# Kernel tuning notes

Measured on AMD Instinct MI355X. Metric: run time of the kernel, lower is better.

The kernel has to match this reference:

```python
import jax, jax.numpy as jnp
import numpy as np

N_NODES = 100000


def high_pass_filter(z, src, dst, n):
    # add self loops (PyG add_self_loops appends [i, i] edges)
    loop = jnp.arange(n, dtype=src.dtype)
    src2 = jnp.concatenate([src, loop])
    dst2 = jnp.concatenate([dst, loop])
    ones = jnp.ones(src2.shape[0], dtype=z.dtype)
    # deg = degree(edge_index[0]) -> out-degree counts per source node
    deg = jax.ops.segment_sum(ones, src2, num_segments=n)
    # mean aggregation at target nodes: out[i] = mean_{(j->i)} z[j]
    msg_sum = jax.ops.segment_sum(z[src2], dst2, num_segments=n)
    cnt = jax.ops.segment_sum(ones, dst2, num_segments=n)
    mean_out = msg_sum / cnt[:, None]  # cnt >= 1 thanks to self loops
    return z - mean_out / deg[:, None]


def setup_inputs() -> dict:
    key = jax.random.key(0)
    k = jax.random.split(key, 8)
    d = 64
    E = 1200000
    x = jax.random.normal(k[0], (N_NODES, d), dtype=jnp.float32)
    edge_index = jax.random.randint(k[1], (2, E), 0, N_NODES, dtype=jnp.int64)
    s = 1.0 / np.sqrt(d)
    W1 = jax.random.uniform(k[2], (d, d), jnp.float32, -s, s)
    b1 = jax.random.uniform(k[3], (d,), jnp.float32, -s, s)
    W2 = jax.random.uniform(k[4], (d, d), jnp.float32, -s, s)
    b2 = jax.random.uniform(k[5], (d,), jnp.float32, -s, s)
    W3 = jax.random.uniform(k[6], (d, d), jnp.float32, -s, s)
    b3 = jax.random.uniform(k[7], (d,), jnp.float32, -s, s)
    return {"x": x, "edge_index": edge_index, "W1": W1, "b1": b1,
            "W2": W2, "b2": b2, "W3": W3, "b3": b3}


def reference(x, edge_index, W1, b1, W2, b2, W3, b3):
    src, dst = edge_index[0], edge_index[1]
    n = x.shape[0]
    z = jax.nn.relu(x @ W1 + b1)
    z = high_pass_filter(z, src, dst, n)
    z = jax.nn.relu(z @ W2 + b2)
    z = high_pass_filter(z, src, dst, n)
    z = jax.nn.relu(z @ W3 + b3)
    return z
```

## Files before the change

kernel.cpp:

```cpp
#include <hip/hip_runtime.h>

#define D 64
#define CAP 48
#define CAPB 3584
#define BIN_CHUNK 2048

typedef unsigned int uint;
typedef unsigned short ushort;

__device__ __forceinline__ ushort f2bf(float f) {
    uint u = __float_as_uint(f);
    return (ushort)((u + 0x7FFFu + ((u >> 16) & 1u)) >> 16);
}

__global__ __launch_bounds__(256) void k_bin2(
    const int* __restrict__ src, const int* __restrict__ dst, int E, int nb,
    int* __restrict__ gcur, int* __restrict__ binD, int* __restrict__ binS)
{
    __shared__ int curD[512], curS[512];
    const int t = threadIdx.x;
    for (int i = t; i < nb; i += 256) { curD[i] = 0; curS[i] = 0; }
    __syncthreads();

    const int e0 = blockIdx.x * BIN_CHUNK;
    int sv[8], dv[8];
#pragma unroll
    for (int i = 0; i < 8; ++i) {
        int e = e0 + i * 256 + t;
        if (e < E) {
            sv[i] = src[e]; dv[i] = dst[e];
            atomicAdd(&curD[dv[i] >> 8], 1);
            atomicAdd(&curS[sv[i] >> 8], 1);
        } else {
            sv[i] = -1;
        }
    }
    __syncthreads();
    for (int i = t; i < nb; i += 256) {
        int c = curD[i]; curD[i] = c ? atomicAdd(&gcur[i], c) : 0;
        c = curS[i];     curS[i] = c ? atomicAdd(&gcur[nb + i], c) : 0;
    }
    __syncthreads();
#pragma unroll
    for (int i = 0; i < 8; ++i) {
        if (sv[i] >= 0) {
            int b = dv[i] >> 8;
            int pos = atomicAdd(&curD[b], 1);
            if (pos < CAPB) binD[(size_t)b * CAPB + pos] = ((dv[i] & 255) << 17) | sv[i];
            b = sv[i] >> 8;
            pos = atomicAdd(&curS[b], 1);
            if (pos < CAPB) binS[(size_t)b * CAPB + pos] = sv[i] & 255;
        }
    }
}

__global__ __launch_bounds__(256) void k_finish(
    const int* __restrict__ gcur, const int* __restrict__ binD,
    const int* __restrict__ binS, int n, int nb,
    int* __restrict__ csr, int* __restrict__ icnt, float* __restrict__ inv)
{
    __shared__ int cur[256], od[256];
    const int b = blockIdx.x, t = threadIdx.x;
    cur[t] = 0; od[t] = 0;
    __syncthreads();

    int cntD = gcur[b]; if (cntD > CAPB) cntD = CAPB;
    const int* bb = binD + (size_t)b * CAPB;
    for (int i = t; i < cntD; i += 256) {
        int v = bb[i];
        int dloc = v >> 17;
        int pos = atomicAdd(&cur[dloc], 1);
        if (pos < CAP) csr[(size_t)((b << 8) + dloc) * CAP + pos] = v & 0x1FFFF;
    }
    int cntS = gcur[nb + b]; if (cntS > CAPB) cntS = CAPB;
    const int* bs = binS + (size_t)b * CAPB;
    for (int i = t; i < cntS; i += 256) {
        atomicAdd(&od[bs[i]], 1);
    }
    __syncthreads();
    int node = (b << 8) + t;
    if (node < n) {
        int ic = cur[t]; if (ic > CAP) ic = CAP;
        icnt[node] = ic;
        inv[node] = 1.0f / ((float)(od[t] + 1) * (float)(ic + 1));
    }
}

__global__ __launch_bounds__(256) void k_aggr(
    const float* __restrict__ zA, const ushort* __restrict__ zh,
    const int* __restrict__ icnt, const int* __restrict__ csr,
    const float* __restrict__ inv, int n, float* __restrict__ zB)
{
    int w = (blockIdx.x * 256 + threadIdx.x) >> 6;
    int lane = threadIdx.x & 63;
    int c8 = (lane & 7) << 3;
    int j = lane >> 3;
    if (w >= n) return;

    int cnt = icnt[w]; if (cnt > CAP) cnt = CAP;
    int rs = w * CAP;
    float a[8] = {0.f, 0.f, 0.f, 0.f, 0.f, 0.f, 0.f, 0.f};
    for (int e = rs + j; e < rs + cnt; e += 8) {
        int s = csr[e];
        uint4 u = *(const uint4*)(zh + (size_t)s * D + c8);
        a[0] += __uint_as_float(u.x << 16);
        a[1] += __uint_as_float(u.x & 0xFFFF0000u);
        a[2] += __uint_as_float(u.y << 16);
        a[3] += __uint_as_float(u.y & 0xFFFF0000u);
        a[4] += __uint_as_float(u.z << 16);
        a[5] += __uint_as_float(u.z & 0xFFFF0000u);
        a[6] += __uint_as_float(u.w << 16);
        a[7] += __uint_as_float(u.w & 0xFFFF0000u);
    }
#pragma unroll
    for (int m = 8; m <= 32; m <<= 1) {
#pragma unroll
        for (int i = 0; i < 8; ++i) a[i] += __shfl_xor(a[i], m, 64);
    }

    if (j == 0) {
        float iv = inv[w];
        const float* zr = zA + (size_t)w * D + c8;
        float4 s0 = *(const float4*)zr;
        float4 s1 = *(const float4*)(zr + 4);
        float4 o0, o1;
        o0.x = fmaf(-(a[0] + s0.x), iv, s0.x);
        o0.y = fmaf(-(a[1] + s0.y), iv, s0.y);
        o0.z = fmaf(-(a[2] + s0.z), iv, s0.z);
        o0.w = fmaf(-(a[3] + s0.w), iv, s0.w);
        o1.x = fmaf(-(a[4] + s1.x), iv, s1.x);
        o1.y = fmaf(-(a[5] + s1.y), iv, s1.y);
        o1.z = fmaf(-(a[6] + s1.z), iv, s1.z);
        o1.w = fmaf(-(a[7] + s1.w), iv, s1.w);
        float* zo = zB + (size_t)w * D + c8;
        *(float4*)zo = o0;
        *(float4*)(zo + 4) = o1;
    }
}

#define LDS_STRIDE 68

__global__ __launch_bounds__(256) void k_gemm(
    const float* z, const float* __restrict__ W, const float* __restrict__ bias,
    float* out, ushort* zh_out, int n)
{
    __shared__ float sX[64 * LDS_STRIDE];
    __shared__ float sWT[64 * LDS_STRIDE];

    const int t = threadIdx.x;
    const int row0 = blockIdx.x * 64;

    for (int i = 0; i < 4; ++i) {
        int s = i * 256 + t;
        int k = s >> 4;
        int c4 = (s & 15) << 2;
        float4 w = ((const float4*)W)[s];
        sWT[(c4 + 0) * LDS_STRIDE + k] = w.x;
        sWT[(c4 + 1) * LDS_STRIDE + k] = w.y;
        sWT[(c4 + 2) * LDS_STRIDE + k] = w.z;
        sWT[(c4 + 3) * LDS_STRIDE + k] = w.w;
    }
    for (int i = 0; i < 4; ++i) {
        int s = i * 256 + t;
        int r = s >> 4;
        int grow = row0 + r;
        float4 v = make_float4(0.f, 0.f, 0.f, 0.f);
        if (grow < n) v = ((const float4*)(z + (size_t)grow * D))[s & 15];
        *((float4*)(sX + r * LDS_STRIDE + ((s & 15) << 2))) = v;
    }
    __syncthreads();

    const int tc = (t & 15) << 2;
    const int tr = (t >> 4) << 2;

    float acc[4][4] = {};
#define DOT4(a_, w_, acc_) \
    acc_ = fmaf((a_).x, (w_).x, fmaf((a_).y, (w_).y, fmaf((a_).z, (w_).z, fmaf((a_).w, (w_).w, acc_))))

    for (int k4 = 0; k4 < 16; ++k4) {
        float4 a0 = *(const float4*)(sX + (tr + 0) * LDS_STRIDE + (k4 << 2));
        float4 a1 = *(const float4*)(sX + (tr + 1) * LDS_STRIDE + (k4 << 2));
        float4 a2 = *(const float4*)(sX + (tr + 2) * LDS_STRIDE + (k4 << 2));
        float4 a3 = *(const float4*)(sX + (tr + 3) * LDS_STRIDE + (k4 << 2));
        float4 w0 = *(const float4*)(sWT + (tc + 0) * LDS_STRIDE + (k4 << 2));
        float4 w1 = *(const float4*)(sWT + (tc + 1) * LDS_STRIDE + (k4 << 2));
        float4 w2 = *(const float4*)(sWT + (tc + 2) * LDS_STRIDE + (k4 << 2));
        float4 w3 = *(const float4*)(sWT + (tc + 3) * LDS_STRIDE + (k4 << 2));
        DOT4(a0, w0, acc[0][0]); DOT4(a0, w1, acc[0][1]); DOT4(a0, w2, acc[0][2]); DOT4(a0, w3, acc[0][3]);
        DOT4(a1, w0, acc[1][0]); DOT4(a1, w1, acc[1][1]); DOT4(a1, w2, acc[1][2]); DOT4(a1, w3, acc[1][3]);
        DOT4(a2, w0, acc[2][0]); DOT4(a2, w1, acc[2][1]); DOT4(a2, w2, acc[2][2]); DOT4(a2, w3, acc[2][3]);
        DOT4(a3, w0, acc[3][0]); DOT4(a3, w1, acc[3][1]); DOT4(a3, w2, acc[3][2]); DOT4(a3, w3, acc[3][3]);
    }

    float b0 = bias[tc + 0], b1 = bias[tc + 1], b2 = bias[tc + 2], b3 = bias[tc + 3];
    for (int rr = 0; rr < 4; ++rr) {
        int grow = row0 + tr + rr;
        if (grow >= n) continue;
        float4 o;
        o.x = fmaxf(acc[rr][0] + b0, 0.f);
        o.y = fmaxf(acc[rr][1] + b1, 0.f);
        o.z = fmaxf(acc[rr][2] + b2, 0.f);
        o.w = fmaxf(acc[rr][3] + b3, 0.f);
        ((float4*)(out + (size_t)grow * D))[tc >> 2] = o;
        if (zh_out) {
            short4 h;
            h.x = (short)f2bf(o.x); h.y = (short)f2bf(o.y);
            h.z = (short)f2bf(o.z); h.w = (short)f2bf(o.w);
            *(short4*)(zh_out + (size_t)grow * D + tc) = h;
        }
    }
}

extern "C" void kernel_launch(void* const* d_in, const int* in_sizes, int n_in,
                              void* d_out, int out_size, void* d_ws, size_t ws_size,
                              hipStream_t stream) {
    const float* x  = (const float*)d_in[0];
    const int*   ei = (const int*)d_in[1];
    const float* W1 = (const float*)d_in[2];
    const float* b1 = (const float*)d_in[3];
    const float* W2 = (const float*)d_in[4];
    const float* b2 = (const float*)d_in[5];
    const float* W3 = (const float*)d_in[6];
    const float* b3 = (const float*)d_in[7];

    const int n = in_sizes[0] / D;
    const int E = in_sizes[1] / 2;
    const int* src = ei;
    const int* dst = ei + E;

    const int nb = (n + 255) >> 8;

    float*  zA   = (float*)d_ws;
    ushort* zh   = (ushort*)(zA + (size_t)n * D);
    float*  inv  = (float*)(zh + (size_t)n * D);
    int*    icnt = (int*)(inv + n);
    int*    csr  = icnt + n;
    int*    gcur = csr + (size_t)n * CAP;
    int*    binD = gcur + 2 * nb;
    int*    binS = binD + (size_t)nb * CAPB;

    float* out = (float*)d_out;
    dim3 blk(256);

    hipMemsetAsync(gcur, 0, 2 * (size_t)nb * sizeof(int), stream);

    const int bin_blocks = (E + BIN_CHUNK - 1) / BIN_CHUNK;
    k_bin2<<<dim3(bin_blocks), blk, 0, stream>>>(src, dst, E, nb, gcur, binD, binS);
    k_finish<<<dim3(nb), blk, 0, stream>>>(gcur, binD, binS, n, nb, csr, icnt, inv);

    dim3 gemm_grid((n + 63) / 64);
    dim3 aggr_grid((n + 3) / 4);

    k_gemm<<<gemm_grid, blk, 0, stream>>>(x, W1, b1, zA, zh, n);
    k_aggr<<<aggr_grid, blk, 0, stream>>>(zA, zh, icnt, csr, inv, n, zA);
    k_gemm<<<gemm_grid, blk, 0, stream>>>(zA, W2, b2, zA, zh, n);
    k_aggr<<<aggr_grid, blk, 0, stream>>>(zA, zh, icnt, csr, inv, n, zA);
    k_gemm<<<gemm_grid, blk, 0, stream>>>(zA, W3, b3, out, nullptr, n);
}
```

Before: 296.2 us.

## Fuse all phases into one persistent cooperative kernel with grid syncs

Replaces the memset and seven separate kernel launches (binning, CSR finish, three GEMMs, two aggregations) with a single cooperative persistent kernel. Blocks loop over work items and phases are separated by grid-wide syncs. The aim is to remove launch overhead and inter-kernel gaps. In exchange, occupancy is capped at the computed resident-block count, grid.sync adds its own cost, and the GEMM tiles may get less latency hiding than with oversubscribed grids.

```diff
diff --git a/kernel.cpp b/kernel.cpp
--- a/kernel.cpp
+++ b/kernel.cpp
@@ -1,9 +1,13 @@
 #include <hip/hip_runtime.h>
+#include <hip/hip_cooperative_groups.h>
+
+namespace cg = cooperative_groups;
 
 #define D 64
 #define CAP 48
 #define CAPB 3584
 #define BIN_CHUNK 2048
+#define LDS_STRIDE 68
 
 typedef unsigned int uint;
 typedef unsigned short ushort;
@@ -13,142 +17,142 @@
     return (ushort)((u + 0x7FFFu + ((u >> 16) & 1u)) >> 16);
 }
 
-__global__ __launch_bounds__(256) void k_bin2(
-    const int* __restrict__ src, const int* __restrict__ dst, int E, int nb,
-    int* __restrict__ gcur, int* __restrict__ binD, int* __restrict__ binS)
-{
-    __shared__ int curD[512], curS[512];
+__device__ void phase_bin(const int* __restrict__ src, const int* __restrict__ dst,
+                          int E, int nb, int* __restrict__ gcur,
+                          int* __restrict__ binD, int* __restrict__ binS, int* shm)
+{
+    int* curD = shm;
+    int* curS = shm + 512;
     const int t = threadIdx.x;
-    for (int i = t; i < nb; i += 256) { curD[i] = 0; curS[i] = 0; }
-    __syncthreads();
-
-    const int e0 = blockIdx.x * BIN_CHUNK;
-    int sv[8], dv[8];
-#pragma unroll
-    for (int i = 0; i < 8; ++i) {
-        int e = e0 + i * 256 + t;
-        if (e < E) {
-            sv[i] = src[e]; dv[i] = dst[e];
-            atomicAdd(&curD[dv[i] >> 8], 1);
-            atomicAdd(&curS[sv[i] >> 8], 1);
-        } else {
-            sv[i] = -1;
-        }
-    }
-    __syncthreads();
-    for (int i = t; i < nb; i += 256) {
-        int c = curD[i]; curD[i] = c ? atomicAdd(&gcur[i], c) : 0;
-        c = curS[i];     curS[i] = c ? atomicAdd(&gcur[nb + i], c) : 0;
-    }
-    __syncthreads();
-#pragma unroll
-    for (int i = 0; i < 8; ++i) {
-        if (sv[i] >= 0) {
-            int b = dv[i] >> 8;
-            int pos = atomicAdd(&curD[b], 1);
-            if (pos < CAPB) binD[(size_t)b * CAPB + pos] = ((dv[i] & 255) << 17) | sv[i];
-            b = sv[i] >> 8;
-            pos = atomicAdd(&curS[b], 1);
-            if (pos < CAPB) binS[(size_t)b * CAPB + pos] = sv[i] & 255;
-        }
-    }
-}
-
-__global__ __launch_bounds__(256) void k_finish(
-    const int* __restrict__ gcur, const int* __restrict__ binD,
-    const int* __restrict__ binS, int n, int nb,
-    int* __restrict__ csr, int* __restrict__ icnt, float* __restrict__ inv)
-{
-    __shared__ int cur[256], od[256];
-    const int b = blockIdx.x, t = threadIdx.x;
-    cur[t] = 0; od[t] = 0;
-    __syncthreads();
-
-    int cntD = gcur[b]; if (cntD > CAPB) cntD = CAPB;
-    const int* bb = binD + (size_t)b * CAPB;
-    for (int i = t; i < cntD; i += 256) {
-        int v = bb[i];
-        int dloc = v >> 17;
-        int pos = atomicAdd(&cur[dloc], 1);
-        if (pos < CAP) csr[(size_t)((b << 8) + dloc) * CAP + pos] = v & 0x1FFFF;
-    }
-    int cntS = gcur[nb + b]; if (cntS > CAPB) cntS = CAPB;
-    const int* bs = binS + (size_t)b * CAPB;
-    for (int i = t; i < cntS; i += 256) {
-        atomicAdd(&od[bs[i]], 1);
-    }
-    __syncthreads();
-    int node = (b << 8) + t;
-    if (node < n) {
-        int ic = cur[t]; if (ic > CAP) ic = CAP;
-        icnt[node] = ic;
-        inv[node] = 1.0f / ((float)(od[t] + 1) * (float)(ic + 1));
-    }
-}
-
-__global__ __launch_bounds__(256) void k_aggr(
-    const float* __restrict__ zA, const ushort* __restrict__ zh,
-    const int* __restrict__ icnt, const int* __restrict__ csr,
-    const float* __restrict__ inv, int n, float* __restrict__ zB)
-{
-    int w = (blockIdx.x * 256 + threadIdx.x) >> 6;
-    int lane = threadIdx.x & 63;
-    int c8 = (lane & 7) << 3;
-    int j = lane >> 3;
-    if (w >= n) return;
-
-    int cnt = icnt[w]; if (cnt > CAP) cnt = CAP;
-    int rs = w * CAP;
-    float a[8] = {0.f, 0.f, 0.f, 0.f, 0.f, 0.f, 0.f, 0.f};
-    for (int e = rs + j; e < rs + cnt; e += 8) {
-        int s = csr[e];
-        uint4 u = *(const uint4*)(zh + (size_t)s * D + c8);
-        a[0] += __uint_as_float(u.x << 16);
-        a[1] += __uint_as_float(u.x & 0xFFFF0000u);
-        a[2] += __uint_as_float(u.y << 16);
-        a[3] += __uint_as_float(u.y & 0xFFFF0000u);
-        a[4] += __uint_as_float(u.z << 16);
-        a[5] += __uint_as_float(u.z & 0xFFFF0000u);
-        a[6] += __uint_as_float(u.w << 16);
-        a[7] += __uint_as_float(u.w & 0xFFFF0000u);
-    }
-#pragma unroll
-    for (int m = 8; m <= 32; m <<= 1) {
-#pragma unroll
-        for (int i = 0; i < 8; ++i) a[i] += __shfl_xor(a[i], m, 64);
-    }
-
-    if (j == 0) {
-        float iv = inv[w];
-        const float* zr = zA + (size_t)w * D + c8;
-        float4 s0 = *(const float4*)zr;
-        float4 s1 = *(const float4*)(zr + 4);
-        float4 o0, o1;
-        o0.x = fmaf(-(a[0] + s0.x), iv, s0.x);
-        o0.y = fmaf(-(a[1] + s0.y), iv, s0.y);
-        o0.z = fmaf(-(a[2] + s0.z), iv, s0.z);
-        o0.w = fmaf(-(a[3] + s0.w), iv, s0.w);
-        o1.x = fmaf(-(a[4] + s1.x), iv, s1.x);
-        o1.y = fmaf(-(a[5] + s1.y), iv, s1.y);
-        o1.z = fmaf(-(a[6] + s1.z), iv, s1.z);
-        o1.w = fmaf(-(a[7] + s1.w), iv, s1.w);
-        float* zo = zB + (size_t)w * D + c8;
-        *(float4*)zo = o0;
-        *(float4*)(zo + 4) = o1;
-    }
-}
-
-#define LDS_STRIDE 68
-
-__global__ __launch_bounds__(256) void k_gemm(
-    const float* z, const float* __restrict__ W, const float* __restrict__ bias,
-    float* out, ushort* zh_out, int n)
-{
-    __shared__ float sX[64 * LDS_STRIDE];
-    __shared__ float sWT[64 * LDS_STRIDE];
-
+    const int nchunks = (E + BIN_CHUNK - 1) / BIN_CHUNK;
+    for (int c = blockIdx.x; c < nchunks; c += gridDim.x) {
+        for (int i = t; i < nb; i += 256) { curD[i] = 0; curS[i] = 0; }
+        __syncthreads();
+        const int e0 = c * BIN_CHUNK;
+        int sv[8], dv[8];
+#pragma unroll
+        for (int i = 0; i < 8; ++i) {
+            int e = e0 + i * 256 + t;
+            if (e < E) {
+                sv[i] = src[e]; dv[i] = dst[e];
+                atomicAdd(&curD[dv[i] >> 8], 1);
+                atomicAdd(&curS[sv[i] >> 8], 1);
+            } else {
+                sv[i] = -1;
+            }
+        }
+        __syncthreads();
+        for (int i = t; i < nb; i += 256) {
+            int cc = curD[i]; curD[i] = cc ? atomicAdd(&gcur[i], cc) : 0;
+            cc = curS[i];     curS[i] = cc ? atomicAdd(&gcur[nb + i], cc) : 0;
+        }
+        __syncthreads();
+#pragma unroll
+        for (int i = 0; i < 8; ++i) {
+            if (sv[i] >= 0) {
+                int b = dv[i] >> 8;
+                int pos = atomicAdd(&curD[b], 1);
+                if (pos < CAPB) binD[(size_t)b * CAPB + pos] = ((dv[i] & 255) << 17) | sv[i];
+                b = sv[i] >> 8;
+                pos = atomicAdd(&curS[b], 1);
+                if (pos < CAPB) binS[(size_t)b * CAPB + pos] = sv[i] & 255;
+            }
+        }
+        __syncthreads();
+    }
+}
+
+__device__ void phase_finish(const int* __restrict__ gcur, const int* __restrict__ binD,
+                             const int* __restrict__ binS, int n, int nb,
+                             int* __restrict__ csr, int* __restrict__ icnt,
+                             float* __restrict__ inv, int* shm)
+{
+    int* cur = shm;
+    int* od  = shm + 256;
     const int t = threadIdx.x;
-    const int row0 = blockIdx.x * 64;
+    for (int b = blockIdx.x; b < nb; b += gridDim.x) {
+        cur[t] = 0; od[t] = 0;
+        __syncthreads();
+        int cntD = gcur[b]; if (cntD > CAPB) cntD = CAPB;
+        const int* bb = binD + (size_t)b * CAPB;
+        for (int i = t; i < cntD; i += 256) {
+            int v = bb[i];
+            int dloc = v >> 17;
+            int pos = atomicAdd(&cur[dloc], 1);
+            if (pos < CAP) csr[(size_t)((b << 8) + dloc) * CAP + pos] = v & 0x1FFFF;
+        }
+        int cntS = gcur[nb + b]; if (cntS > CAPB) cntS = CAPB;
+        const int* bs = binS + (size_t)b * CAPB;
+        for (int i = t; i < cntS; i += 256) atomicAdd(&od[bs[i]], 1);
+        __syncthreads();
+        int node = (b << 8) + t;
+        if (node < n) {
+            int ic = cur[t]; if (ic > CAP) ic = CAP;
+            icnt[node] = ic;
+            inv[node] = 1.0f / ((float)(od[t] + 1) * (float)(ic + 1));
+        }
+        __syncthreads();
+    }
+}
+
+__device__ void phase_aggr(const float* __restrict__ zA, const ushort* __restrict__ zh,
+                           const int* __restrict__ icnt, const int* __restrict__ csr,
+                           const float* __restrict__ inv, int n, float* __restrict__ zB)
+{
+    const int lane = threadIdx.x & 63;
+    const int c8 = (lane & 7) << 3;
+    const int j = lane >> 3;
+    const int wave0 = (blockIdx.x * 256 + threadIdx.x) >> 6;
+    const int nwaves = gridDim.x << 2;
+    for (int w = wave0; w < n; w += nwaves) {
+        int cnt = icnt[w]; if (cnt > CAP) cnt = CAP;
+        int rs = w * CAP;
+        float a[8] = {0.f, 0.f, 0.f, 0.f, 0.f, 0.f, 0.f, 0.f};
+        for (int e = rs + j; e < rs + cnt; e += 8) {
+            int s = csr[e];
+            uint4 u = *(const uint4*)(zh + (size_t)s * D + c8);
+            a[0] += __uint_as_float(u.x << 16);
+            a[1] += __uint_as_float(u.x & 0xFFFF0000u);
+            a[2] += __uint_as_float(u.y << 16);
+            a[3] += __uint_as_float(u.y & 0xFFFF0000u);
+            a[4] += __uint_as_float(u.z << 16);
+            a[5] += __uint_as_float(u.z & 0xFFFF0000u);
+            a[6] += __uint_as_float(u.w << 16);
+            a[7] += __uint_as_float(u.w & 0xFFFF0000u);
+        }
+#pragma unroll
+        for (int m = 8; m <= 32; m <<= 1) {
+#pragma unroll
+            for (int i = 0; i < 8; ++i) a[i] += __shfl_xor(a[i], m, 64);
+        }
+        if (j == 0) {
+            float iv = inv[w];
+            const float* zr = zA + (size_t)w * D + c8;
+            float4 s0 = *(const float4*)zr;
+            float4 s1 = *(const float4*)(zr + 4);
+            float4 o0, o1;
+            o0.x = fmaf(-(a[0] + s0.x), iv, s0.x);
+            o0.y = fmaf(-(a[1] + s0.y), iv, s0.y);
+            o0.z = fmaf(-(a[2] + s0.z), iv, s0.z);
+            o0.w = fmaf(-(a[3] + s0.w), iv, s0.w);
+            o1.x = fmaf(-(a[4] + s1.x), iv, s1.x);
+            o1.y = fmaf(-(a[5] + s1.y), iv, s1.y);
+            o1.z = fmaf(-(a[6] + s1.z), iv, s1.z);
+            o1.w = fmaf(-(a[7] + s1.w), iv, s1.w);
+            float* zo = zB + (size_t)w * D + c8;
+            *(float4*)zo = o0;
+            *(float4*)(zo + 4) = o1;
+        }
+    }
+}
+
+__device__ void phase_gemm(const float* z, const float* __restrict__ W,
+                           const float* __restrict__ bias, float* out,
+                           ushort* zh_out, int n, float* smem)
+{
+    float* sX  = smem;
+    float* sWT = smem + 64 * LDS_STRIDE;
+    const int t = threadIdx.x;
 
     for (int i = 0; i < 4; ++i) {
         int s = i * 256 + t;
@@ -160,55 +164,89 @@
         sWT[(c4 + 2) * LDS_STRIDE + k] = w.z;
         sWT[(c4 + 3) * LDS_STRIDE + k] = w.w;
     }
-    for (int i = 0; i < 4; ++i) {
-        int s = i * 256 + t;
-        int r = s >> 4;
-        int grow = row0 + r;
-        float4 v = make_float4(0.f, 0.f, 0.f, 0.f);
-        if (grow < n) v = ((const float4*)(z + (size_t)grow * D))[s & 15];
-        *((float4*)(sX + r * LDS_STRIDE + ((s & 15) << 2))) = v;
-    }
-    __syncthreads();
 
     const int tc = (t & 15) << 2;
     const int tr = (t >> 4) << 2;
-
-    float acc[4][4] = {};
+    float b0 = bias[tc + 0], b1 = bias[tc + 1], b2 = bias[tc + 2], b3 = bias[tc + 3];
+
+    const int ntiles = (n + 63) >> 6;
+    for (int tile = blockIdx.x; tile < ntiles; tile += gridDim.x) {
+        const int row0 = tile << 6;
+        for (int i = 0; i < 4; ++i) {
+            int s = i * 256 + t;
+            int r = s >> 4;
+            int grow = row0 + r;
+            float4 v = make_float4(0.f, 0.f, 0.f, 0.f);
+            if (grow < n) v = ((const float4*)(z + (size_t)grow * D))[s & 15];
+            *((float4*)(sX + r * LDS_STRIDE + ((s & 15) << 2))) = v;
+        }
+        __syncthreads();
+
+        float acc[4][4] = {};
 #define DOT4(a_, w_, acc_) \
     acc_ = fmaf((a_).x, (w_).x, fmaf((a_).y, (w_).y, fmaf((a_).z, (w_).z, fmaf((a_).w, (w_).w, acc_))))
-
-    for (int k4 = 0; k4 < 16; ++k4) {
-        float4 a0 = *(const float4*)(sX + (tr + 0) * LDS_STRIDE + (k4 << 2));
-        float4 a1 = *(const float4*)(sX + (tr + 1) * LDS_STRIDE + (k4 << 2));
-        float4 a2 = *(const float4*)(sX + (tr + 2) * LDS_STRIDE + (k4 << 2));
-        float4 a3 = *(const float4*)(sX + (tr + 3) * LDS_STRIDE + (k4 << 2));
-        float4 w0 = *(const float4*)(sWT + (tc + 0) * LDS_STRIDE + (k4 << 2));
-        float4 w1 = *(const float4*)(sWT + (tc + 1) * LDS_STRIDE + (k4 << 2));
-        float4 w2 = *(const float4*)(sWT + (tc + 2) * LDS_STRIDE + (k4 << 2));
-        float4 w3 = *(const float4*)(sWT + (tc + 3) * LDS_STRIDE + (k4 << 2));
-        DOT4(a0, w0, acc[0][0]); DOT4(a0, w1, acc[0][1]); DOT4(a0, w2, acc[0][2]); DOT4(a0, w3, acc[0][3]);
-        DOT4(a1, w0, acc[1][0]); DOT4(a1, w1, acc[1][1]); DOT4(a1, w2, acc[1][2]); DOT4(a1, w3, acc[1][3]);
-        DOT4(a2, w0, acc[2][0]); DOT4(a2, w1, acc[2][1]); DOT4(a2, w2, acc[2][2]); DOT4(a2, w3, acc[2][3]);
-        DOT4(a3, w0, acc[3][0]); DOT4(a3, w1, acc[3][1]); DOT4(a3, w2, acc[3][2]); DOT4(a3, w3, acc[3][3]);
-    }
-
-    float b0 = bias[tc + 0], b1 = bias[tc + 1], b2 = bias[tc + 2], b3 = bias[tc + 3];
-    for (int rr = 0; rr < 4; ++rr) {
-        int grow = row0 + tr + rr;
-        if (grow >= n) continue;
-        float4 o;
-        o.x = fmaxf(acc[rr][0] + b0, 0.f);
-        o.y = fmaxf(acc[rr][1] + b1, 0.f);
-        o.z = fmaxf(acc[rr][2] + b2, 0.f);
-        o.w = fmaxf(acc[rr][3] + b3, 0.f);
-        ((float4*)(out + (size_t)grow * D))[tc >> 2] = o;
-        if (zh_out) {
-            short4 h;
-            h.x = (short)f2bf(o.x); h.y = (short)f2bf(o.y);
-            h.z = (short)f2bf(o.z); h.w = (short)f2bf(o.w);
-            *(short4*)(zh_out + (size_t)grow * D + tc) = h;
-        }
-    }
+        for (int k4 = 0; k4 < 16; ++k4) {
+            float4 a0 = *(const float4*)(sX + (tr + 0) * LDS_STRIDE + (k4 << 2));
+            float4 a1 = *(const float4*)(sX + (tr + 1) * LDS_STRIDE + (k4 << 2));
+            float4 a2 = *(const float4*)(sX + (tr + 2) * LDS_STRIDE + (k4 << 2));
+            float4 a3 = *(const float4*)(sX + (tr + 3) * LDS_STRIDE + (k4 << 2));
+            float4 w0 = *(const float4*)(sWT + (tc + 0) * LDS_STRIDE + (k4 << 2));
+            float4 w1 = *(const float4*)(sWT + (tc + 1) * LDS_STRIDE + (k4 << 2));
+            float4 w2 = *(const float4*)(sWT + (tc + 2) * LDS_STRIDE + (k4 << 2));
+            float4 w3 = *(const float4*)(sWT + (tc + 3) * LDS_STRIDE + (k4 << 2));
+            DOT4(a0, w0, acc[0][0]); DOT4(a0, w1, acc[0][1]); DOT4(a0, w2, acc[0][2]); DOT4(a0, w3, acc[0][3]);
+            DOT4(a1, w0, acc[1][0]); DOT4(a1, w1, acc[1][1]); DOT4(a1, w2, acc[1][2]); DOT4(a1, w3, acc[1][3]);
+            DOT4(a2, w0, acc[2][0]); DOT4(a2, w1, acc[2][1]); DOT4(a2, w2, acc[2][2]); DOT4(a2, w3, acc[2][3]);
+            DOT4(a3, w0, acc[3][0]); DOT4(a3, w1, acc[3][1]); DOT4(a3, w2, acc[3][2]); DOT4(a3, w3, acc[3][3]);
+        }
+#undef DOT4
+
+        for (int rr = 0; rr < 4; ++rr) {
+            int grow = row0 + tr + rr;
+            if (grow >= n) continue;
+            float4 o;
+            o.x = fmaxf(acc[rr][0] + b0, 0.f);
+            o.y = fmaxf(acc[rr][1] + b1, 0.f);
+            o.z = fmaxf(acc[rr][2] + b2, 0.f);
+            o.w = fmaxf(acc[rr][3] + b3, 0.f);
+            ((float4*)(out + (size_t)grow * D))[tc >> 2] = o;
+            if (zh_out) {
+                short4 h;
+                h.x = (short)f2bf(o.x); h.y = (short)f2bf(o.y);
+                h.z = (short)f2bf(o.z); h.w = (short)f2bf(o.w);
+                *(short4*)(zh_out + (size_t)grow * D + tc) = h;
+            }
+        }
+        __syncthreads();
+    }
+}
+
+__global__ __launch_bounds__(256) void k_fused(
+    const float* x, const int* src, const int* dst,
+    const float* W1, const float* b1, const float* W2, const float* b2,
+    const float* W3, const float* b3, float* out,
+    float* zA, ushort* zh, float* inv, int* icnt, int* csr, int* gcur,
+    int* binD, int* binS, int n, int E, int nb)
+{
+    __shared__ float smem[2 * 64 * LDS_STRIDE];
+    cg::grid_group grid = cg::this_grid();
+
+    for (int i = blockIdx.x * 256 + threadIdx.x; i < 2 * nb; i += gridDim.x * 256)
+        gcur[i] = 0;
+    grid.sync();
+    phase_bin(src, dst, E, nb, gcur, binD, binS, (int*)smem);
+    grid.sync();
+    phase_finish(gcur, binD, binS, n, nb, csr, icnt, inv, (int*)smem);
+    grid.sync();
+    phase_gemm(x, W1, b1, zA, zh, n, smem);
+    grid.sync();
+    phase_aggr(zA, zh, icnt, csr, inv, n, zA);
+    grid.sync();
+    phase_gemm(zA, W2, b2, zA, zh, n, smem);
+    grid.sync();
+    phase_aggr(zA, zh, icnt, csr, inv, n, zA);
+    grid.sync();
+    phase_gemm(zA, W3, b3, out, nullptr, n, smem);
 }
 
 extern "C" void kernel_launch(void* const* d_in, const int* in_sizes, int n_in,
@@ -227,7 +265,6 @@
     const int E = in_sizes[1] / 2;
     const int* src = ei;
     const int* dst = ei + E;
-
     const int nb = (n + 255) >> 8;
 
     float*  zA   = (float*)d_ws;
@@ -240,20 +277,19 @@
     int*    binS = binD + (size_t)nb * CAPB;
 
     float* out = (float*)d_out;
-    dim3 blk(256);
-
-    hipMemsetAsync(gcur, 0, 2 * (size_t)nb * sizeof(int), stream);
-
-    const int bin_blocks = (E + BIN_CHUNK - 1) / BIN_CHUNK;
-    k_bin2<<<dim3(bin_blocks), blk, 0, stream>>>(src, dst, E, nb, gcur, binD, binS);
-    k_finish<<<dim3(nb), blk, 0, stream>>>(gcur, binD, binS, n, nb, csr, icnt, inv);
-
-    dim3 gemm_grid((n + 63) / 64);
-    dim3 aggr_grid((n + 3) / 4);
-
-    k_gemm<<<gemm_grid, blk, 0, stream>>>(x, W1, b1, zA, zh, n);
-    k_aggr<<<aggr_grid, blk, 0, stream>>>(zA, zh, icnt, csr, inv, n, zA);
-    k_gemm<<<gemm_grid, blk, 0, stream>>>(zA, W2, b2, zA, zh, n);
-    k_aggr<<<aggr_grid, blk, 0, stream>>>(zA, zh, icnt, csr, inv, n, zA);
-    k_gemm<<<gemm_grid, blk, 0, stream>>>(zA, W3, b3, out, nullptr, n);
-}
+
+    int perCU = 0;
+    hipOccupancyMaxActiveBlocksPerMultiprocessor(&perCU, k_fused, 256, 0);
+    if (perCU < 1) perCU = 1;
+    int grid = perCU * 256;
+
+    void* args[] = {
+        (void*)&x, (void*)&src, (void*)&dst,
+        (void*)&W1, (void*)&b1, (void*)&W2, (void*)&b2, (void*)&W3, (void*)&b3,
+        (void*)&out,
+        (void*)&zA, (void*)&zh, (void*)&inv, (void*)&icnt, (void*)&csr,
+        (void*)&gcur, (void*)&binD, (void*)&binS,
+        (void*)&n, (void*)&E, (void*)&nb
+    };
+    hipLaunchCooperativeKernel(k_fused, dim3(grid), dim3(256), args, 0, stream);
+}
```

Measured after the change: 815.9 us. 2.75x slower.
